# Performance work log

Hardware: AMD Instinct MI355X
Metric: run time of the kernel (lower is better)

The kernel has to match this reference:

```python
import jax, jax.numpy as jnp
import numpy as np

S, B, I, H = 1024, 128, 256, 256


def setup_inputs() -> dict:
    key = jax.random.key(0)
    ks = jax.random.split(key, 9)
    w = 0.05  # small init scale for numerical stability
    d = {"x": jax.random.normal(ks[0], (S, B, I), jnp.float32)}
    names = [("Wxi", "Whi", "bxi", "bhi"), ("Wxf", "Whf", "bxf", "bhf"),
             ("Wxo", "Who", "bxo", "bho"), ("Wxc", "Whc", "bxc", "bhc")]
    for gi, (wx, wh, bx, bh) in enumerate(names):
        d[wx] = jax.random.normal(ks[1 + 2 * gi], (H, I), jnp.float32) * w
        d[wh] = jax.random.normal(ks[2 + 2 * gi], (H, H), jnp.float32) * w
        d[bx] = jnp.zeros((H,), jnp.float32)
        d[bh] = jnp.zeros((H,), jnp.float32)
    return d


def reference(x, Wxi, bxi, Whi, bhi, Wxf, bxf, Whf, bhf,
              Wxo, bxo, Who, bho, Wxc, bxc, Whc, bhc):
    # Precompute all input-to-hidden projections in one batched GEMM per gate
    # (mathematically identical to per-step Linear on xt).
    xi = jnp.einsum('sbi,hi->sbh', x, Wxi) + bxi
    xf = jnp.einsum('sbi,hi->sbh', x, Wxf) + bxf
    xo = jnp.einsum('sbi,hi->sbh', x, Wxo) + bxo
    xc = jnp.einsum('sbi,hi->sbh', x, Wxc) + bxc

    Bsz = x.shape[1]
    h0 = jnp.zeros((Bsz, Wxi.shape[0]), x.dtype)
    c0 = jnp.zeros_like(h0)

    def step(carry, gates_t):
        h, c = carry
        gi, gf, go, gc = gates_t
        i = jax.nn.sigmoid(gi + h @ Whi.T + bhi)
        f = jax.nn.sigmoid(gf + h @ Whf.T + bhf)
        o = jax.nn.sigmoid(go + h @ Who.T + bho)
        g = jnp.tanh(gc + h @ Whc.T + bhc)
        c = f * c + i * g
        h = o * jnp.tanh(c)
        return (h, c), h

    (h, c), h_seq = jax.lax.scan(step, (h0, c0), (xi, xf, xo, xc))
    return h_seq, (h[None], c[None])
```

## Files before the change

kernel.cpp:

```cpp
#include <hip/hip_runtime.h>
#include <hip/hip_bf16.h>

#define S_LEN 1024
#define BATCH 128
#define HDIM  256
#define IDIM  256


__global__ __launch_bounds__(512) void lstm_persist(
    const float* __restrict__ x,
    const float* __restrict__ Wxi, const float* __restrict__ Whi,
    const float* __restrict__ bxi, const float* __restrict__ bhi,
    const float* __restrict__ Wxf, const float* __restrict__ Whf,
    const float* __restrict__ bxf, const float* __restrict__ bhf,
    const float* __restrict__ Wxo, const float* __restrict__ Who,
    const float* __restrict__ bxo, const float* __restrict__ bho,
    const float* __restrict__ Wxc, const float* __restrict__ Whc,
    const float* __restrict__ bxc, const float* __restrict__ bhc,
    float* __restrict__ out,
    float* __restrict__ hslot,
    unsigned int* __restrict__ flags)
{
  const int bid = blockIdx.x;
  const int bg  = bid & 31;
  const int hs  = bid >> 5;
  const int tid = threadIdx.x;
  const int hh  = tid >> 4;
  const int kq  = tid & 15;
  const int b0  = bg * 4;

  int col4[4];
#pragma unroll
  for (int j = 0; j < 4; ++j) col4[j] = kq * 16 + 4 * (((kq >> 1) + j) & 3);

  float wh[4][16], wx[4][16];
#pragma unroll
  for (int r = 0; r < 4; ++r) {
    const int ghrow = hh * 4 + r;
    const int g     = ghrow >> 5;
    const int hrow  = hs * 32 + (ghrow & 31);
    const float* Whp = (g == 0) ? Whi : (g == 1) ? Whf : (g == 2) ? Who : Whc;
    const float* Wxp = (g == 0) ? Wxi : (g == 1) ? Wxf : (g == 2) ? Wxo : Wxc;
#pragma unroll
    for (int j = 0; j < 4; ++j) {
      float4 a = *(const float4*)(Whp + (size_t)hrow * HDIM + col4[j]);
      wh[r][4*j+0] = a.x; wh[r][4*j+1] = a.y; wh[r][4*j+2] = a.z; wh[r][4*j+3] = a.w;
      float4 c = *(const float4*)(Wxp + (size_t)hrow * IDIM + col4[j]);
      wx[r][4*j+0] = c.x; wx[r][4*j+1] = c.y; wx[r][4*j+2] = c.z; wx[r][4*j+3] = c.w;
    }
  }

  const int cb  = tid >> 5;
  const int ch2 = tid & 31;
  const int chrow = hs * 32 + ch2;
  const float bias_i = bxi[chrow] + bhi[chrow];
  const float bias_f = bxf[chrow] + bhf[chrow];
  const float bias_o = bxo[chrow] + bho[chrow];
  const float bias_c = bxc[chrow] + bhc[chrow];

  const int srow = tid >> 7;
  const int scol = (tid & 127) * 2;

  __shared__ float h_lds[4][HDIM];
  __shared__ float pre_lds[4][129];

  float acc[16];

  {
    const float* xb = x + (size_t)b0 * IDIM;
#pragma unroll
    for (int i = 0; i < 16; ++i) acc[i] = 0.f;
#pragma unroll
    for (int j = 0; j < 4; ++j)
#pragma unroll
      for (int b = 0; b < 4; ++b) {
        float4 v = *(const float4*)(xb + b * IDIM + col4[j]);
#pragma unroll
        for (int r = 0; r < 4; ++r)
          acc[b + 4*r] += wx[r][4*j+0]*v.x + wx[r][4*j+1]*v.y
                        + wx[r][4*j+2]*v.z + wx[r][4*j+3]*v.w;
      }
  }

  float creg = 0.f, hreg = 0.f;

  for (int t = 0; t < S_LEN; ++t) {
    if (tid < 8) {
      const unsigned tgt = (unsigned)t;
      long cnt = 0;
      while (__hip_atomic_load(&flags[(tid * 32 + bg) * 16], __ATOMIC_RELAXED,
                               __HIP_MEMORY_SCOPE_AGENT) < tgt) {
        if (++cnt > 50000000L) break;
      }
    }
    __syncthreads();

    {
      const float* src = hslot + (size_t)((t & 1) ^ 1) * BATCH * HDIM
                       + (size_t)(b0 + srow) * HDIM + scol;
      unsigned long long u = __hip_atomic_load(
          (const unsigned long long*)src, __ATOMIC_RELAXED,
          __HIP_MEMORY_SCOPE_AGENT);
      h_lds[srow][scol]     = __uint_as_float((unsigned)u);
      h_lds[srow][scol + 1] = __uint_as_float((unsigned)(u >> 32));
    }
    __syncthreads();

#pragma unroll
    for (int j = 0; j < 4; ++j)
#pragma unroll
      for (int b = 0; b < 4; ++b) {
        const float4 v = *(const float4*)&h_lds[b][col4[j]];
#pragma unroll
        for (int r = 0; r < 4; ++r)
          acc[b + 4*r] += wh[r][4*j+0]*v.x + wh[r][4*j+1]*v.y
                        + wh[r][4*j+2]*v.z + wh[r][4*j+3]*v.w;
      }

    float s;
    {
      float a8[8];
      { const int bit = kq & 1;
#pragma unroll
        for (int j = 0; j < 8; ++j) {
          float keep = bit ? acc[2*j+1] : acc[2*j];
          float send = bit ? acc[2*j]   : acc[2*j+1];
          a8[j] = keep + __shfl_xor(send, 1);
        } }
      float a4[4];
      { const int bit = (kq >> 1) & 1;
#pragma unroll
        for (int j = 0; j < 4; ++j) {
          float keep = bit ? a8[2*j+1] : a8[2*j];
          float send = bit ? a8[2*j]   : a8[2*j+1];
          a4[j] = keep + __shfl_xor(send, 2);
        } }
      float a2[2];
      { const int bit = (kq >> 2) & 1;
#pragma unroll
        for (int j = 0; j < 2; ++j) {
          float keep = bit ? a4[2*j+1] : a4[2*j];
          float send = bit ? a4[2*j]   : a4[2*j+1];
          a2[j] = keep + __shfl_xor(send, 4);
        } }
      { const int bit = (kq >> 3) & 1;
        float keep = bit ? a2[1] : a2[0];
        float send = bit ? a2[0] : a2[1];
        s = keep + __shfl_xor(send, 8);
      }
    }
    pre_lds[kq & 3][hh * 4 + (kq >> 2)] = s;
    __syncthreads();

    if (tid < 128) {
      float gi = pre_lds[cb][0*32 + ch2] + bias_i;
      float gf = pre_lds[cb][1*32 + ch2] + bias_f;
      float go = pre_lds[cb][2*32 + ch2] + bias_o;
      float gc = pre_lds[cb][3*32 + ch2] + bias_c;
      float ig = 1.f / (1.f + expf(-gi));
      float fg = 1.f / (1.f + expf(-gf));
      float og = 1.f / (1.f + expf(-go));
      float cg = tanhf(gc);
      creg = fg * creg + ig * cg;
      hreg = og * tanhf(creg);
      const int bgl = b0 + cb;
      __hip_atomic_store(
          &hslot[(size_t)(t & 1) * BATCH * HDIM + (size_t)bgl * HDIM + chrow],
          hreg, __ATOMIC_RELAXED, __HIP_MEMORY_SCOPE_AGENT);
      out[(size_t)t * BATCH * HDIM + (size_t)bgl * HDIM + chrow] = hreg;
    }
    __syncthreads();
    if (tid == 0) {
      __hip_atomic_store(&flags[bid * 16], (unsigned)(t + 1), __ATOMIC_RELAXED,
                         __HIP_MEMORY_SCOPE_AGENT);
    }

    {
      const int tn = (t + 1 < S_LEN) ? (t + 1) : (S_LEN - 1);
      const float* xb = x + ((size_t)tn * BATCH + b0) * IDIM;
#pragma unroll
      for (int i = 0; i < 16; ++i) acc[i] = 0.f;
#pragma unroll
      for (int j = 0; j < 4; ++j)
#pragma unroll
        for (int b = 0; b < 4; ++b) {
          float4 v = *(const float4*)(xb + b * IDIM + col4[j]);
#pragma unroll
          for (int r = 0; r < 4; ++r)
            acc[b + 4*r] += wx[r][4*j+0]*v.x + wx[r][4*j+1]*v.y
                          + wx[r][4*j+2]*v.z + wx[r][4*j+3]*v.w;
        }
    }
  }

  if (tid < 128) {
    float* oh = out + (size_t)S_LEN * BATCH * HDIM;
    const int bgl = b0 + cb;
    oh[(size_t)bgl * HDIM + chrow] = hreg;
    oh[(size_t)BATCH * HDIM + (size_t)bgl * HDIM + chrow] = creg;
  }
}

extern "C" void kernel_launch(void* const* d_in, const int* in_sizes, int n_in,
                              void* d_out, int out_size, void* d_ws, size_t ws_size,
                              hipStream_t stream) {
  const float* x   = (const float*)d_in[0];
  const float* Wxi = (const float*)d_in[1];
  const float* Whi = (const float*)d_in[2];
  const float* bxi = (const float*)d_in[3];
  const float* bhi = (const float*)d_in[4];
  const float* Wxf = (const float*)d_in[5];
  const float* Whf = (const float*)d_in[6];
  const float* bxf = (const float*)d_in[7];
  const float* bhf = (const float*)d_in[8];
  const float* Wxo = (const float*)d_in[9];
  const float* Who = (const float*)d_in[10];
  const float* bxo = (const float*)d_in[11];
  const float* bho = (const float*)d_in[12];
  const float* Wxc = (const float*)d_in[13];
  const float* Whc = (const float*)d_in[14];
  const float* bxc = (const float*)d_in[15];
  const float* bhc = (const float*)d_in[16];

  float* out = (float*)d_out;
  float* hslot = (float*)d_ws;
  unsigned int* flags =
      (unsigned int*)((char*)d_ws + (size_t)2 * BATCH * HDIM * sizeof(float));

  hipMemsetAsync(d_ws, 0,
                 (size_t)2 * BATCH * HDIM * sizeof(float) +
                     (size_t)256 * 16 * sizeof(unsigned int),
                 stream);

  lstm_persist<<<dim3(256), dim3(512), 0, stream>>>(
      x, Wxi, Whi, bxi, bhi, Wxf, Whf, bxf, bhf,
      Wxo, Who, bxo, bho, Wxc, Whc, bxc, bhc,
      out, hslot, flags);
}
```

Measured before the change: 7.447 ms.

## Split LSTM recurrence across 512 blocks with 16 hidden rows each

Repartitions the persistent LSTM kernel from 256 blocks (32 hidden units per block) to 512 blocks (16 hidden units per block). Each thread now holds one gate row with 32 weights per matrix instead of four rows with 16, so the per-step dot product and the shuffle reduction get shorter. The intent is to cut per-step latency on the serial critical path. The output store is also moved after the flag publish, and launch bounds now request 4 blocks per CU. In exchange, each block polls 16 peer flags instead of 8 and the total block count doubles, which adds synchronisation traffic and relies on all 512 blocks being co-resident for the spin-wait scheme to work.

```diff
diff --git a/kernel.cpp b/kernel.cpp
--- a/kernel.cpp
+++ b/kernel.cpp
@@ -7,7 +7,7 @@
 #define IDIM  256
 
 
-__global__ __launch_bounds__(512) void lstm_persist(
+__global__ __launch_bounds__(512, 4) void lstm_persist(
     const float* __restrict__ x,
     const float* __restrict__ Wxi, const float* __restrict__ Whi,
     const float* __restrict__ bxi, const float* __restrict__ bhi,
@@ -22,37 +22,34 @@
     unsigned int* __restrict__ flags)
 {
   const int bid = blockIdx.x;
-  const int bg  = bid & 31;
-  const int hs  = bid >> 5;
+  const int bg  = bid >> 4;
+  const int hsl = bid & 15;
   const int tid = threadIdx.x;
-  const int hh  = tid >> 4;
-  const int kq  = tid & 15;
+  const int row = tid >> 3;
+  const int ks  = tid & 7;
   const int b0  = bg * 4;
 
-  int col4[4];
-#pragma unroll
-  for (int j = 0; j < 4; ++j) col4[j] = kq * 16 + 4 * (((kq >> 1) + j) & 3);
-
-  float wh[4][16], wx[4][16];
-#pragma unroll
-  for (int r = 0; r < 4; ++r) {
-    const int ghrow = hh * 4 + r;
-    const int g     = ghrow >> 5;
-    const int hrow  = hs * 32 + (ghrow & 31);
-    const float* Whp = (g == 0) ? Whi : (g == 1) ? Whf : (g == 2) ? Who : Whc;
-    const float* Wxp = (g == 0) ? Wxi : (g == 1) ? Wxf : (g == 2) ? Wxo : Wxc;
-#pragma unroll
-    for (int j = 0; j < 4; ++j) {
-      float4 a = *(const float4*)(Whp + (size_t)hrow * HDIM + col4[j]);
-      wh[r][4*j+0] = a.x; wh[r][4*j+1] = a.y; wh[r][4*j+2] = a.z; wh[r][4*j+3] = a.w;
-      float4 c = *(const float4*)(Wxp + (size_t)hrow * IDIM + col4[j]);
-      wx[r][4*j+0] = c.x; wx[r][4*j+1] = c.y; wx[r][4*j+2] = c.z; wx[r][4*j+3] = c.w;
-    }
-  }
-
-  const int cb  = tid >> 5;
-  const int ch2 = tid & 31;
-  const int chrow = hs * 32 + ch2;
+  int col8[8];
+#pragma unroll
+  for (int j = 0; j < 8; ++j) col8[j] = ks * 32 + 4 * ((ks + j) & 7);
+
+  const int g    = row >> 4;
+  const int h16r = row & 15;
+  const int hrow = hsl * 16 + h16r;
+  const float* Whp = (g == 0) ? Whi : (g == 1) ? Whf : (g == 2) ? Who : Whc;
+  const float* Wxp = (g == 0) ? Wxi : (g == 1) ? Wxf : (g == 2) ? Wxo : Wxc;
+  float wh[32], wx[32];
+#pragma unroll
+  for (int j = 0; j < 8; ++j) {
+    float4 a = *(const float4*)(Whp + (size_t)hrow * HDIM + col8[j]);
+    wh[4*j+0] = a.x; wh[4*j+1] = a.y; wh[4*j+2] = a.z; wh[4*j+3] = a.w;
+    float4 c = *(const float4*)(Wxp + (size_t)hrow * IDIM + col8[j]);
+    wx[4*j+0] = c.x; wx[4*j+1] = c.y; wx[4*j+2] = c.z; wx[4*j+3] = c.w;
+  }
+
+  const int cb   = tid >> 4;
+  const int ch16 = tid & 15;
+  const int chrow = hsl * 16 + ch16;
   const float bias_i = bxi[chrow] + bhi[chrow];
   const float bias_f = bxf[chrow] + bhf[chrow];
   const float bias_o = bxo[chrow] + bho[chrow];
@@ -62,33 +59,30 @@
   const int scol = (tid & 127) * 2;
 
   __shared__ float h_lds[4][HDIM];
-  __shared__ float pre_lds[4][129];
-
-  float acc[16];
+  __shared__ float pre_lds[4][65];
+
+  float acc[4];
 
   {
     const float* xb = x + (size_t)b0 * IDIM;
 #pragma unroll
-    for (int i = 0; i < 16; ++i) acc[i] = 0.f;
-#pragma unroll
-    for (int j = 0; j < 4; ++j)
+    for (int b = 0; b < 4; ++b) acc[b] = 0.f;
+#pragma unroll
+    for (int j = 0; j < 8; ++j)
 #pragma unroll
       for (int b = 0; b < 4; ++b) {
-        float4 v = *(const float4*)(xb + b * IDIM + col4[j]);
-#pragma unroll
-        for (int r = 0; r < 4; ++r)
-          acc[b + 4*r] += wx[r][4*j+0]*v.x + wx[r][4*j+1]*v.y
-                        + wx[r][4*j+2]*v.z + wx[r][4*j+3]*v.w;
+        float4 v = *(const float4*)(xb + b * IDIM + col8[j]);
+        acc[b] += wx[4*j+0]*v.x + wx[4*j+1]*v.y + wx[4*j+2]*v.z + wx[4*j+3]*v.w;
       }
   }
 
   float creg = 0.f, hreg = 0.f;
 
   for (int t = 0; t < S_LEN; ++t) {
-    if (tid < 8) {
+    if (tid < 16) {
       const unsigned tgt = (unsigned)t;
       long cnt = 0;
-      while (__hip_atomic_load(&flags[(tid * 32 + bg) * 16], __ATOMIC_RELAXED,
+      while (__hip_atomic_load(&flags[(bg * 16 + tid) * 16], __ATOMIC_RELAXED,
                                __HIP_MEMORY_SCOPE_AGENT) < tgt) {
         if (++cnt > 50000000L) break;
       }
@@ -107,67 +101,47 @@
     __syncthreads();
 
 #pragma unroll
-    for (int j = 0; j < 4; ++j)
+    for (int j = 0; j < 8; ++j)
 #pragma unroll
       for (int b = 0; b < 4; ++b) {
-        const float4 v = *(const float4*)&h_lds[b][col4[j]];
-#pragma unroll
-        for (int r = 0; r < 4; ++r)
-          acc[b + 4*r] += wh[r][4*j+0]*v.x + wh[r][4*j+1]*v.y
-                        + wh[r][4*j+2]*v.z + wh[r][4*j+3]*v.w;
+        const float4 v = *(const float4*)&h_lds[b][col8[j]];
+        acc[b] += wh[4*j+0]*v.x + wh[4*j+1]*v.y + wh[4*j+2]*v.z + wh[4*j+3]*v.w;
       }
 
     float s;
     {
-      float a8[8];
-      { const int bit = kq & 1;
-#pragma unroll
-        for (int j = 0; j < 8; ++j) {
+      float a2[2];
+      { const int bit = ks & 1;
+#pragma unroll
+        for (int j = 0; j < 2; ++j) {
           float keep = bit ? acc[2*j+1] : acc[2*j];
           float send = bit ? acc[2*j]   : acc[2*j+1];
-          a8[j] = keep + __shfl_xor(send, 1);
+          a2[j] = keep + __shfl_xor(send, 1);
         } }
-      float a4[4];
-      { const int bit = (kq >> 1) & 1;
-#pragma unroll
-        for (int j = 0; j < 4; ++j) {
-          float keep = bit ? a8[2*j+1] : a8[2*j];
-          float send = bit ? a8[2*j]   : a8[2*j+1];
-          a4[j] = keep + __shfl_xor(send, 2);
-        } }
-      float a2[2];
-      { const int bit = (kq >> 2) & 1;
-#pragma unroll
-        for (int j = 0; j < 2; ++j) {
-          float keep = bit ? a4[2*j+1] : a4[2*j];
-          float send = bit ? a4[2*j]   : a4[2*j+1];
-          a2[j] = keep + __shfl_xor(send, 4);
-        } }
-      { const int bit = (kq >> 3) & 1;
+      { const int bit = (ks >> 1) & 1;
         float keep = bit ? a2[1] : a2[0];
         float send = bit ? a2[0] : a2[1];
-        s = keep + __shfl_xor(send, 8);
-      }
-    }
-    pre_lds[kq & 3][hh * 4 + (kq >> 2)] = s;
-    __syncthreads();
-
-    if (tid < 128) {
-      float gi = pre_lds[cb][0*32 + ch2] + bias_i;
-      float gf = pre_lds[cb][1*32 + ch2] + bias_f;
-      float go = pre_lds[cb][2*32 + ch2] + bias_o;
-      float gc = pre_lds[cb][3*32 + ch2] + bias_c;
+        s = keep + __shfl_xor(send, 2);
+      }
+      s += __shfl_xor(s, 4);
+    }
+    if (ks < 4) pre_lds[ks][row] = s;
+    __syncthreads();
+
+    if (tid < 64) {
+      float gi = pre_lds[cb][0*16 + ch16] + bias_i;
+      float gf = pre_lds[cb][1*16 + ch16] + bias_f;
+      float go = pre_lds[cb][2*16 + ch16] + bias_o;
+      float gc = pre_lds[cb][3*16 + ch16] + bias_c;
       float ig = 1.f / (1.f + expf(-gi));
       float fg = 1.f / (1.f + expf(-gf));
       float og = 1.f / (1.f + expf(-go));
       float cg = tanhf(gc);
       creg = fg * creg + ig * cg;
       hreg = og * tanhf(creg);
-      const int bgl = b0 + cb;
       __hip_atomic_store(
-          &hslot[(size_t)(t & 1) * BATCH * HDIM + (size_t)bgl * HDIM + chrow],
+          &hslot[(size_t)(t & 1) * BATCH * HDIM + (size_t)(b0 + cb) * HDIM + chrow],
           hreg, __ATOMIC_RELAXED, __HIP_MEMORY_SCOPE_AGENT);
-      out[(size_t)t * BATCH * HDIM + (size_t)bgl * HDIM + chrow] = hreg;
     }
     __syncthreads();
     if (tid == 0) {
@@ -175,29 +149,29 @@
                          __HIP_MEMORY_SCOPE_AGENT);
     }
 
+    if (tid < 64) {
+      out[(size_t)t * BATCH * HDIM + (size_t)(b0 + cb) * HDIM + chrow] = hreg;
+    }
+
     {
       const int tn = (t + 1 < S_LEN) ? (t + 1) : (S_LEN - 1);
       const float* xb = x + ((size_t)tn * BATCH + b0) * IDIM;
 #pragma unroll
-      for (int i = 0; i < 16; ++i) acc[i] = 0.f;
-#pragma unroll
-      for (int j = 0; j < 4; ++j)
+      for (int b = 0; b < 4; ++b) acc[b] = 0.f;
+#pragma unroll
+      for (int j = 0; j < 8; ++j)
 #pragma unroll
         for (int b = 0; b < 4; ++b) {
-          float4 v = *(const float4*)(xb + b * IDIM + col4[j]);
-#pragma unroll
-          for (int r = 0; r < 4; ++r)
-            acc[b + 4*r] += wx[r][4*j+0]*v.x + wx[r][4*j+1]*v.y
-                          + wx[r][4*j+2]*v.z + wx[r][4*j+3]*v.w;
+          float4 v = *(const float4*)(xb + b * IDIM + col8[j]);
+          acc[b] += wx[4*j+0]*v.x + wx[4*j+1]*v.y + wx[4*j+2]*v.z + wx[4*j+3]*v.w;
         }
     }
   }
 
-  if (tid < 128) {
+  if (tid < 64) {
     float* oh = out + (size_t)S_LEN * BATCH * HDIM;
-    const int bgl = b0 + cb;
-    oh[(size_t)bgl * HDIM + chrow] = hreg;
-    oh[(size_t)BATCH * HDIM + (size_t)bgl * HDIM + chrow] = creg;
+    oh[(size_t)(b0 + cb) * HDIM + chrow] = hreg;
+    oh[(size_t)BATCH * HDIM + (size_t)(b0 + cb) * HDIM + chrow] = creg;
   }
 }
 
@@ -229,10 +203,10 @@
 
   hipMemsetAsync(d_ws, 0,
                  (size_t)2 * BATCH * HDIM * sizeof(float) +
-                     (size_t)256 * 16 * sizeof(unsigned int),
+                     (size_t)512 * 16 * sizeof(unsigned int),
                  stream);
 
-  lstm_persist<<<dim3(256), dim3(512), 0, stream>>>(
+  lstm_persist<<<dim3(512), dim3(512), 0, stream>>>(
       x, Wxi, Whi, bxi, bhi, Wxf, Whf, bxf, bhf,
       Wxo, Who, bxo, bho, Wxc, Whc, bxc, bhc,
       out, hslot, flags);
```

Result: slower. 21.31 ms (+186.2%).

## Pack timestep tag with hidden value to replace per-block flag barrier

Applied to the files above, without the earlier changes.

Each hidden-state element is now stored as a 64-bit word that pairs the float with its timestep tag. Consumers spin directly on the data words they need, so the flag polling, one __syncthreads and the separate flag store are gone. The goal is to cut the cross-block synchronisation latency on every recurrent step. In exchange the workspace doubles in size and every thread polls global memory. Correctness now depends on each 64-bit atomic store being seen whole, and the ping-pong slot reuse still relies on the tags rising monotonically.

```diff
diff --git a/kernel.cpp b/kernel.cpp
--- a/kernel.cpp
+++ b/kernel.cpp
@@ -18,8 +18,7 @@
     const float* __restrict__ Wxc, const float* __restrict__ Whc,
     const float* __restrict__ bxc, const float* __restrict__ bhc,
     float* __restrict__ out,
-    float* __restrict__ hslot,
-    unsigned int* __restrict__ flags)
+    unsigned long long* __restrict__ hpair)
 {
   const int bid = blockIdx.x;
   const int bg  = bid & 31;
@@ -85,24 +84,21 @@
   float creg = 0.f, hreg = 0.f;
 
   for (int t = 0; t < S_LEN; ++t) {
-    if (tid < 8) {
-      const unsigned tgt = (unsigned)t;
+    {
+      const unsigned long long* p0 = hpair
+          + (size_t)((t & 1) ^ 1) * BATCH * HDIM
+          + (size_t)(b0 + srow) * HDIM + scol;
+      const unsigned tg = (unsigned)t;
+      unsigned long long u0, u1;
       long cnt = 0;
-      while (__hip_atomic_load(&flags[(tid * 32 + bg) * 16], __ATOMIC_RELAXED,
-                               __HIP_MEMORY_SCOPE_AGENT) < tgt) {
-        if (++cnt > 50000000L) break;
-      }
-    }
-    __syncthreads();
-
-    {
-      const float* src = hslot + (size_t)((t & 1) ^ 1) * BATCH * HDIM
-                       + (size_t)(b0 + srow) * HDIM + scol;
-      unsigned long long u = __hip_atomic_load(
-          (const unsigned long long*)src, __ATOMIC_RELAXED,
-          __HIP_MEMORY_SCOPE_AGENT);
-      h_lds[srow][scol]     = __uint_as_float((unsigned)u);
-      h_lds[srow][scol + 1] = __uint_as_float((unsigned)(u >> 32));
+      for (;;) {
+        u0 = __hip_atomic_load(p0,     __ATOMIC_RELAXED, __HIP_MEMORY_SCOPE_AGENT);
+        u1 = __hip_atomic_load(p0 + 1, __ATOMIC_RELAXED, __HIP_MEMORY_SCOPE_AGENT);
+        if (((unsigned)(u0 >> 32) >= tg) & ((unsigned)(u1 >> 32) >= tg)) break;
+        if (++cnt > 20000000L) break;
+      }
+      h_lds[srow][scol]     = __uint_as_float((unsigned)u0);
+      h_lds[srow][scol + 1] = __uint_as_float((unsigned)u1);
     }
     __syncthreads();
 
@@ -164,15 +160,13 @@
       creg = fg * creg + ig * cg;
       hreg = og * tanhf(creg);
       const int bgl = b0 + cb;
+      const unsigned long long u =
+          ((unsigned long long)(unsigned)(t + 1) << 32) |
+          (unsigned long long)__float_as_uint(hreg);
       __hip_atomic_store(
-          &hslot[(size_t)(t & 1) * BATCH * HDIM + (size_t)bgl * HDIM + chrow],
-          hreg, __ATOMIC_RELAXED, __HIP_MEMORY_SCOPE_AGENT);
+          &hpair[(size_t)(t & 1) * BATCH * HDIM + (size_t)bgl * HDIM + chrow],
+          u, __ATOMIC_RELAXED, __HIP_MEMORY_SCOPE_AGENT);
       out[(size_t)t * BATCH * HDIM + (size_t)bgl * HDIM + chrow] = hreg;
-    }
-    __syncthreads();
-    if (tid == 0) {
-      __hip_atomic_store(&flags[bid * 16], (unsigned)(t + 1), __ATOMIC_RELAXED,
-                         __HIP_MEMORY_SCOPE_AGENT);
     }
 
     {
@@ -223,17 +217,13 @@
   const float* bhc = (const float*)d_in[16];
 
   float* out = (float*)d_out;
-  float* hslot = (float*)d_ws;
-  unsigned int* flags =
-      (unsigned int*)((char*)d_ws + (size_t)2 * BATCH * HDIM * sizeof(float));
-
-  hipMemsetAsync(d_ws, 0,
-                 (size_t)2 * BATCH * HDIM * sizeof(float) +
-                     (size_t)256 * 16 * sizeof(unsigned int),
+  unsigned long long* hpair = (unsigned long long*)d_ws;
+
+  hipMemsetAsync(d_ws, 0, (size_t)2 * BATCH * HDIM * sizeof(unsigned long long),
                  stream);
 
   lstm_persist<<<dim3(256), dim3(512), 0, stream>>>(
       x, Wxi, Whi, bxi, bhi, Wxf, Whf, bxf, bhf,
       Wxo, Who, bxo, bho, Wxc, Whc, bxc, bhc,
-      out, hslot, flags);
+      out, hpair);
 }
```

After: 8.233 ms. +10.6%, slower.
